# Kernel optimization log

Measured on AMD Instinct MI355X. Metric: run time of the kernel, lower is better.

The kernel has to match this reference:

```python
import jax, jax.numpy as jnp
import numpy as np

D = 512      # d_model
H = 8        # n_head
L = 6        # n_layers
DFF = 2048   # d_inner
V = 10000    # vocab
NPOS = 2048
B, T = 8, 1023
S = 1024     # encoder length


def sinusoid_table(n_position, d_hid):
    pos = np.arange(n_position)[:, None].astype(np.float64)
    i = np.arange(d_hid)[None, :]
    angle = pos / np.power(10000.0, 2 * (i // 2) / d_hid)
    tab = np.zeros((n_position, d_hid))
    tab[:, 0::2] = np.sin(angle[:, 0::2])
    tab[:, 1::2] = np.cos(angle[:, 1::2])
    return jnp.asarray(tab, jnp.float32)


def layer_norm(x, g, b, eps=1e-6):
    m = x.mean(-1, keepdims=True)
    v = x.var(-1, keepdims=True)
    return (x - m) / jnp.sqrt(v + eps) * g + b


def mha(x, kv, wq, wk, wv, wo, g, b, mask):
    # x: [B,Lq,D], kv: [B,Lk,D], mask: [B,Lq|1,Lk] int or None
    Bq, Lq, _ = x.shape
    Lk = kv.shape[1]
    dk = D // H
    q = (x @ wq).reshape(Bq, Lq, H, dk).transpose(0, 2, 1, 3)   # bhqd
    k = (kv @ wk).reshape(Bq, Lk, H, dk).transpose(0, 2, 1, 3)  # bhkd
    v = (kv @ wv).reshape(Bq, Lk, H, dk).transpose(0, 2, 1, 3)
    scores = jnp.einsum('bhqd,bhkd->bhqk', q, k) / jnp.sqrt(jnp.asarray(dk, x.dtype))
    if mask is not None:
        scores = jnp.where(mask[:, None, :, :] == 0, jnp.asarray(-1e9, x.dtype), scores)
    a = jax.nn.softmax(scores, axis=-1)
    o = jnp.einsum('bhqk,bhkd->bhqd', a, v).transpose(0, 2, 1, 3).reshape(Bq, Lq, D)
    o = o @ wo + x  # residual
    return layer_norm(o, g, b)


def ffn(x, w1, b1, w2, b2, g, b):
    h = jax.nn.relu(x @ w1 + b1)
    return layer_norm(h @ w2 + b2 + x, g, b)


def setup_inputs() -> dict:
    key = jax.random.key(0)
    ks = iter(jax.random.split(key, 64))
    sc = 0.02
    inp = {}
    inp['trg_seq'] = jax.random.randint(next(ks), (B, T), 0, V, dtype=jnp.int32)
    # causal mask over decoder length T+1 (1 = attend)
    T1 = T + 1
    inp['trg_mask'] = jnp.tril(jnp.ones((T1, T1), jnp.int32))[None].repeat(B, axis=0)
    inp['enc_output'] = jax.random.normal(next(ks), (B, S, D), jnp.float32)
    inp['src_mask'] = jnp.ones((B, 1, S), jnp.int32)
    inp['emb'] = jax.random.normal(next(ks), (V, D), jnp.float32) * sc
    inp['ln0_g'] = jnp.ones((D,), jnp.float32)
    inp['ln0_b'] = jnp.zeros((D,), jnp.float32)
    for nm in ['wq_s', 'wk_s', 'wv_s', 'wo_s', 'wq_c', 'wk_c', 'wv_c', 'wo_c']:
        inp[nm] = jax.random.normal(next(ks), (L, D, D), jnp.float32) * sc
    for nm in ['ln1_g', 'ln2_g', 'ln3_g']:
        inp[nm] = jnp.ones((L, D), jnp.float32)
    for nm in ['ln1_b', 'ln2_b', 'ln3_b']:
        inp[nm] = jnp.zeros((L, D), jnp.float32)
    inp['w1'] = jax.random.normal(next(ks), (L, D, DFF), jnp.float32) * sc
    inp['b1'] = jnp.zeros((L, DFF), jnp.float32)
    inp['w2'] = jax.random.normal(next(ks), (L, DFF, D), jnp.float32) * sc
    inp['b2'] = jnp.zeros((L, D), jnp.float32)
    return inp


def reference(trg_seq, trg_mask, enc_output, src_mask, emb, ln0_g, ln0_b,
              wq_s, wk_s, wv_s, wo_s, ln1_g, ln1_b,
              wq_c, wk_c, wv_c, wo_c, ln2_g, ln2_b,
              w1, b1, w2, b2, ln3_g, ln3_b):
    Bq, Tq = trg_seq.shape
    tok = emb[trg_seq]                                         # [B,T,D]
    x = jnp.concatenate([jnp.zeros((Bq, 1, D), tok.dtype), tok], axis=1)  # [B,T+1,D]
    x = x + sinusoid_table(NPOS, D)[None, :Tq + 1]
    x = layer_norm(x, ln0_g, ln0_b)
    for l in range(L):
        x = mha(x, x, wq_s[l], wk_s[l], wv_s[l], wo_s[l], ln1_g[l], ln1_b[l], trg_mask)
        x = mha(x, enc_output, wq_c[l], wk_c[l], wv_c[l], wo_c[l], ln2_g[l], ln2_b[l], src_mask)
        x = ffn(x, w1[l], b1[l], w2[l], b2[l], ln3_g[l], ln3_b[l])
    return x
```

## Files before the change

### kernel.cpp

```cpp
#include <hip/hip_runtime.h>
#include <stdint.h>


typedef unsigned short u16;
typedef float floatx4 __attribute__((ext_vector_type(4)));
typedef short short8 __attribute__((ext_vector_type(8)));

__device__ __forceinline__ float b2f(u16 u) {
    union { unsigned int i; float f; } c; c.i = ((unsigned int)u) << 16; return c.f;
}
__device__ __forceinline__ u16 f2b(float f) {
    union { float f; unsigned int i; } c; c.f = f;
    return (u16)((c.i + 0x7FFFu + ((c.i >> 16) & 1u)) >> 16);
}
__device__ __forceinline__ float ldf(const void* p, size_t i, bool is32) {
    return is32 ? ((const float*)p)[i] : b2f(((const u16*)p)[i]);
}
__device__ __forceinline__ void async16(u16* lds, const u16* g) {
    __builtin_amdgcn_global_load_lds(
        (const __attribute__((address_space(1))) unsigned int*)g,
        (__attribute__((address_space(3))) unsigned int*)lds, 16, 0, 0);
}
__device__ __forceinline__ void xcd_remap(int gx, int gy, int& bx, int& by) {
    const int fid = bx + gx * by;
    const int xcd = fid & 7;
    const int i = fid >> 3;
    bx = i % gx;
    by = xcd * (gy >> 3) + i / gx;
}

__global__ __launch_bounds__(256)
void conv_bf16_kernel(const void* __restrict__ src, u16* __restrict__ dst,
                      const u16* __restrict__ probe)
{
    const bool is32 = (probe[0] == 0);
    const size_t off = ((size_t)blockIdx.x * 256 + threadIdx.x) * 4;
    u16 o[4];
    if (is32) {
        float4 f = *(const float4*)((const float*)src + off);
        o[0] = f2b(f.x); o[1] = f2b(f.y); o[2] = f2b(f.z); o[3] = f2b(f.w);
    } else {
        uint2 vv = *(const uint2*)((const u16*)src + off);
        const u16* pv = (const u16*)&vv;
        o[0] = pv[0]; o[1] = pv[1]; o[2] = pv[2]; o[3] = pv[3];
    }
    *(uint2*)&dst[off] = *(uint2*)o;
}

__global__ __launch_bounds__(256)
void transpose_layer_kernel(const void* __restrict__ wq_s, const void* __restrict__ wk_s,
                            const void* __restrict__ wv_s, const void* __restrict__ wo_s,
                            const void* __restrict__ wq_c, const void* __restrict__ wk_c,
                            const void* __restrict__ wv_c, const void* __restrict__ wo_c,
                            const void* __restrict__ w1,   const void* __restrict__ w2,
                            u16* __restrict__ wT, const u16* __restrict__ probe,
                            size_t loff2, size_t loff1)
{
    __shared__ u16 tile[32][33];
    const bool is32 = (probe[0] == 0);
    const int bid = blockIdx.x;
    const int tid = threadIdx.x;
    const void* src; u16* dst; int C, R, tr, tc; size_t loff;
    if (bid < 2048) {
        const int mat = bid >> 8, t = bid & 255;
        R = 512; C = 512; tr = t >> 4; tc = t & 15; loff = loff2;
        const void* tbl[8] = {wq_s, wk_s, wv_s, wo_s, wq_c, wk_c, wv_c, wo_c};
        src = tbl[mat]; dst = wT + (size_t)mat * 262144;
    } else if (bid < 3072) {
        const int t = bid - 2048;
        R = 512; C = 2048; tr = t >> 6; tc = t & 63; loff = loff1;
        src = w1; dst = wT + 2097152;
    } else {
        const int t = bid - 3072;
        R = 2048; C = 512; tr = t >> 4; tc = t & 15; loff = loff1;
        src = w2; dst = wT + 3145728;
    }
    const int r = tid >> 3, c0 = (tid & 7) * 4;
    const size_t off = loff + (size_t)(tr * 32 + r) * C + tc * 32 + c0;
    u16 vals[4];
    if (is32) {
        float4 f = *(const float4*)((const float*)src + off);
        vals[0] = f2b(f.x); vals[1] = f2b(f.y); vals[2] = f2b(f.z); vals[3] = f2b(f.w);
    } else {
        uint2 vv = *(const uint2*)((const u16*)src + off);
        const u16* pv = (const u16*)&vv;
        vals[0] = pv[0]; vals[1] = pv[1]; vals[2] = pv[2]; vals[3] = pv[3];
    }
#pragma unroll
    for (int j = 0; j < 4; j++) tile[r][c0 + j] = vals[j];
    __syncthreads();
    uint2 ov; u16* po = (u16*)&ov;
#pragma unroll
    for (int j = 0; j < 4; j++) po[j] = tile[c0 + j][r];
    *(uint2*)&dst[(size_t)(tc * 32 + r) * R + tr * 32 + c0] = ov;
}

template<int EPI>
__global__ __launch_bounds__(512)
void gemm256(const u16* __restrict__ A, const u16* __restrict__ Bt,
             const void* __restrict__ bias, size_t boff,
             u16* __restrict__ outb, u16* __restrict__ out1, u16* __restrict__ out2,
             const u16* __restrict__ probe, int M, int N, int K)
{
    __shared__ u16 As[2][256 * 64];
    __shared__ u16 Bs[2][256 * 64];
    const int tid = threadIdx.x;
    const int lane = tid & 63;
    const int quad = lane >> 4, cl = lane & 15;
    const int wave = tid >> 6;
    const int wm2 = (wave >> 2) * 128;
    const int wn2 = (wave & 3) * 64;
    int bx = blockIdx.x, by = blockIdx.y;
    xcd_remap(gridDim.x, gridDim.y, bx, by);
    const int m0 = by * 256, n0 = bx * 256;

    floatx4 acc[8][4];
#pragma unroll
    for (int i = 0; i < 8; i++)
#pragma unroll
        for (int j = 0; j < 4; j++)
#pragma unroll
            for (int r = 0; r < 4; r++) acc[i][j][r] = 0.0f;

    const int lrow = lane >> 3;
    const int lcol = ((lane & 7) ^ lrow) * 8;
    const u16* gA = &A [(size_t)(m0 + wave * 8 + lrow) * K + lcol];
    const u16* gB = &Bt[(size_t)(n0 + wave * 8 + lrow) * K + lcol];

    auto stage = [&](int bsel, int k0) {
#pragma unroll
        for (int s = 0; s < 4; s++)
            async16(&As[bsel][(s * 64 + wave * 8) * 64], gA + (size_t)s * 64 * K + k0);
#pragma unroll
        for (int s = 0; s < 4; s++)
            async16(&Bs[bsel][(s * 64 + wave * 8) * 64], gB + (size_t)s * 64 * K + k0);
    };

    const int nkt = K >> 6;
    stage(0, 0);
    stage(1, 64);

    const int c7 = cl & 7;
    for (int t = 0; t < nkt; ++t) {
        const int cur = t & 1;
        if (t == nkt - 1) asm volatile("s_waitcnt vmcnt(0)" ::: "memory");
        else              asm volatile("s_waitcnt vmcnt(8)" ::: "memory");
        __builtin_amdgcn_sched_barrier(0);
        __builtin_amdgcn_s_barrier();

        const u16* Ac = As[cur];
        const u16* Bc = Bs[cur];
#pragma unroll
        for (int kk = 0; kk < 2; kk++) {
            const int gsw = ((kk * 4 + quad) ^ c7) * 8;
            short8 af[8], bf[4];
#pragma unroll
            for (int mi = 0; mi < 8; mi++)
                af[mi] = *(const short8*)&Ac[(wm2 + mi * 16 + cl) * 64 + gsw];
#pragma unroll
            for (int ni = 0; ni < 4; ni++)
                bf[ni] = *(const short8*)&Bc[(wn2 + ni * 16 + cl) * 64 + gsw];
#pragma unroll
            for (int mi = 0; mi < 8; mi++)
#pragma unroll
                for (int ni = 0; ni < 4; ni++)
                    acc[mi][ni] = __builtin_amdgcn_mfma_f32_16x16x32_bf16(af[mi], bf[ni], acc[mi][ni], 0, 0, 0);
        }
        __builtin_amdgcn_s_barrier();
        __builtin_amdgcn_sched_barrier(0);
        if (t + 2 < nkt) stage(cur, (t + 2) * 64);
    }

    if (EPI == 4 || EPI == 5) {
        const int sub = n0 >> 9;
        const int cbase = (n0 & 511) + wn2;
        const bool isV = (EPI == 4) ? (sub == 2) : (sub == 1);
        if (!isV) {
            u16* dst = (sub == 0) ? outb : out1;
#pragma unroll
            for (int mi = 0; mi < 8; mi++)
#pragma unroll
                for (int ni = 0; ni < 4; ni++) {
                    const int c = cbase + ni * 16 + cl;
#pragma unroll
                    for (int r = 0; r < 4; r++)
                        dst[(size_t)(m0 + wm2 + mi * 16 + quad * 4 + r) * 512 + c] = f2b(acc[mi][ni][r]);
                }
        } else {
            u16* dst = (EPI == 4) ? out2 : out1;
#pragma unroll
            for (int mi = 0; mi < 8; mi++) {
                const int row0 = m0 + wm2 + mi * 16 + quad * 4;
                const int b8 = (row0 >> 10) * 8;
                const int key0 = row0 & 1023;
#pragma unroll
                for (int ni = 0; ni < 4; ni++) {
                    const int c = cbase + ni * 16 + cl;
                    u16 pk[4];
#pragma unroll
                    for (int r = 0; r < 4; r++) pk[r] = f2b(acc[mi][ni][r]);
                    const size_t vrow = (size_t)(b8 + (c >> 6)) * 64 + (c & 63);
                    *(uint2*)&dst[vrow * 1024 + key0] = *(uint2*)pk;
                }
            }
        }
        return;
    }

    const bool is32 = (probe[0] == 0);
#pragma unroll
    for (int mi = 0; mi < 8; mi++) {
#pragma unroll
        for (int ni = 0; ni < 4; ni++) {
            const int col = n0 + wn2 + ni * 16 + cl;
            const float bv = ldf(bias, boff + col, is32);
#pragma unroll
            for (int r = 0; r < 4; r++) {
                const int row = m0 + wm2 + mi * 16 + quad * 4 + r;
                float v = acc[mi][ni][r] + bv;
                v = fmaxf(v, 0.0f);
                outb[(size_t)row * N + col] = f2b(v);
            }
        }
    }
}

template<int EPI>
__global__ __launch_bounds__(256)
void gemm_bf16(const u16* __restrict__ A, const u16* __restrict__ Bt,
               const void* __restrict__ bias, size_t boff, float* __restrict__ resid,
               u16* __restrict__ outb, u16* __restrict__ out1, u16* __restrict__ out2,
               const u16* __restrict__ probe, int M, int N, int K)
{
    __shared__ u16 As[3][128 * 32];
    __shared__ u16 Bs[3][128 * 32];
    const int tid = threadIdx.x;
    const int lane = tid & 63;
    const int quad = lane >> 4, cl = lane & 15;
    const int wave = tid >> 6;
    const int wm = (wave >> 1) * 64, wn = (wave & 1) * 64;
    int bx = blockIdx.x, by = blockIdx.y;
    xcd_remap(gridDim.x, gridDim.y, bx, by);
    const int m0 = by * 128, n0 = bx * 128;

    floatx4 acc[4][4];
#pragma unroll
    for (int i = 0; i < 4; i++)
#pragma unroll
        for (int j = 0; j < 4; j++)
#pragma unroll
            for (int r = 0; r < 4; r++) acc[i][j][r] = 0.0f;

    const int srow = tid >> 2;
    const int scol = (((tid & 3) ^ ((srow >> 1) & 3))) * 8;
    const int rslot = (quad ^ ((cl >> 1) & 3)) * 8;
    const int Ksub = K / gridDim.z;
    const int kbeg = blockIdx.z * Ksub, kend = kbeg + Ksub;
    const int nsteps = (kend - kbeg) >> 5;

    const u16* ga0 = &A [(size_t)(m0 + srow) * K + scol];
    const u16* ga1 = &A [(size_t)(m0 + 64 + srow) * K + scol];
    const u16* gb0 = &Bt[(size_t)(n0 + srow) * K + scol];
    const u16* gb1 = &Bt[(size_t)(n0 + 64 + srow) * K + scol];

    auto stage = [&](int bsel, int kk) {
        async16(&As[bsel][wave * 512],        ga0 + kk);
        async16(&As[bsel][2048 + wave * 512], ga1 + kk);
        async16(&Bs[bsel][wave * 512],        gb0 + kk);
        async16(&Bs[bsel][2048 + wave * 512], gb1 + kk);
    };

    stage(0, kbeg);
    if (nsteps > 1) stage(1, kbeg + 32);

    for (int t = 0; t < nsteps; ++t) {
        const int cur = t % 3;
        if (t + 2 < nsteps) stage((t + 2) % 3, kbeg + (t + 2) * 32);
        const int rem = nsteps - 1 - t;
        if (rem >= 2)      asm volatile("s_waitcnt vmcnt(8)" ::: "memory");
        else if (rem == 1) asm volatile("s_waitcnt vmcnt(4)" ::: "memory");
        else               asm volatile("s_waitcnt vmcnt(0)" ::: "memory");
        __builtin_amdgcn_sched_barrier(0);
        __builtin_amdgcn_s_barrier();

        const u16* Ac = As[cur];
        const u16* Bc = Bs[cur];
        short8 af[4], bfr[4];
#pragma unroll
        for (int mi = 0; mi < 4; mi++) af[mi]  = *(const short8*)&Ac[(wm + mi * 16 + cl) * 32 + rslot];
#pragma unroll
        for (int ni = 0; ni < 4; ni++) bfr[ni] = *(const short8*)&Bc[(wn + ni * 16 + cl) * 32 + rslot];
#pragma unroll
        for (int mi = 0; mi < 4; mi++)
#pragma unroll
            for (int ni = 0; ni < 4; ni++)
                acc[mi][ni] = __builtin_amdgcn_mfma_f32_16x16x32_bf16(af[mi], bfr[ni], acc[mi][ni], 0, 0, 0);
        __builtin_amdgcn_s_barrier();
    }

    bool is32 = false;
    if (EPI == 1 || EPI == 2 || EPI == 3) is32 = (probe[0] == 0);
    const bool addbias = (bias != nullptr) && (blockIdx.z == 0);
    float* pslice = (EPI == 3) ? resid + (size_t)blockIdx.z * M * N : resid;
#pragma unroll
    for (int mi = 0; mi < 4; mi++) {
#pragma unroll
        for (int ni = 0; ni < 4; ni++) {
            const int col = n0 + wn + ni * 16 + cl;
#pragma unroll
            for (int r = 0; r < 4; r++) {
                const int row = m0 + wm + mi * 16 + quad * 4 + r;
                float v = acc[mi][ni][r];
                if (EPI == 1) { v += ldf(bias, boff + col, is32); v = fmaxf(v, 0.0f); }
                if (EPI == 2) {
                    if (addbias) v += ldf(bias, boff + col, is32);
                    atomicAdd(&resid[(size_t)row * N + col], v);
                } else if (EPI == 3) {
                    if (addbias) v += ldf(bias, boff + col, is32);
                    pslice[(size_t)row * N + col] = v;
                } else {
                    outb[(size_t)row * N + col] = f2b(v);
                }
            }
        }
    }
}

template<int CAUSAL>
__global__ __launch_bounds__(256)
void attn_kernel(const u16* __restrict__ Q, const u16* __restrict__ Kb,
                 const u16* __restrict__ VT, u16* __restrict__ O)
{
    __shared__ u16 Kt[64][72];
    __shared__ u16 Vt[64][72];
    int qt = blockIdx.x, bh = blockIdx.y;
    xcd_remap(gridDim.x, gridDim.y, qt, bh);
    const int b = bh >> 3, h = bh & 7;
    const int tid = threadIdx.x;
    const int w = tid >> 6;
    const int lane = tid & 63;
    const int quad = lane >> 4, cl = lane & 15;

    const size_t qrow = (size_t)(b * 1024 + qt * 64 + w * 16 + cl) * 512 + h * 64;
    const short8 qf0 = *(const short8*)&Q[qrow + quad * 8];
    const short8 qf1 = *(const short8*)&Q[qrow + 32 + quad * 8];
    const int qg = qt * 64 + w * 16 + cl;

    float lsum = 0.0f;
    floatx4 oacc[4];
#pragma unroll
    for (int nb = 0; nb < 4; nb++)
#pragma unroll
        for (int r = 0; r < 4; r++) oacc[nb][r] = 0.0f;

    const int trow = tid >> 3, tcol = (tid & 7) * 8;
    const int tv = tid & 7;
    const int vm = (tv >> 2) * 32 + (tv & 1) * 16 + ((tv >> 1) & 1) * 4;
    const size_t kbase = (size_t)(b * 1024) * 512 + h * 64;
    const size_t vbase = (size_t)(bh * 64) * 1024;

    const int nkt = CAUSAL ? (qt + 1) : 16;
    uint4 ka0 = *(const uint4*)&Kb[kbase + (size_t)trow * 512 + tcol];
    uint4 ka1 = *(const uint4*)&Kb[kbase + (size_t)(trow + 32) * 512 + tcol];
    uint4 va0 = *(const uint4*)&VT[vbase + (size_t)trow * 1024 + tcol];
    uint4 va1 = *(const uint4*)&VT[vbase + (size_t)(trow + 32) * 1024 + tcol];

    for (int kt = 0; kt < nkt; kt++) {
        *(uint4*)&Kt[trow][tcol]      = ka0;
        *(uint4*)&Kt[trow + 32][tcol] = ka1;
        *(uint2*)&Vt[trow][vm]          = make_uint2(va0.x, va0.y);
        *(uint2*)&Vt[trow][vm + 8]      = make_uint2(va0.z, va0.w);
        *(uint2*)&Vt[trow + 32][vm]     = make_uint2(va1.x, va1.y);
        *(uint2*)&Vt[trow + 32][vm + 8] = make_uint2(va1.z, va1.w);
        if (kt + 1 < nkt) {
            const int k1 = (kt + 1) * 64;
            ka0 = *(const uint4*)&Kb[kbase + (size_t)(k1 + trow) * 512 + tcol];
            ka1 = *(const uint4*)&Kb[kbase + (size_t)(k1 + trow + 32) * 512 + tcol];
            va0 = *(const uint4*)&VT[vbase + (size_t)trow * 1024 + k1 + tcol];
            va1 = *(const uint4*)&VT[vbase + (size_t)(trow + 32) * 1024 + k1 + tcol];
        }
        asm volatile("s_waitcnt lgkmcnt(0)" ::: "memory");
        __builtin_amdgcn_sched_barrier(0);
        __builtin_amdgcn_s_barrier();
        __builtin_amdgcn_sched_barrier(0);

        const int k0 = kt * 64;
        floatx4 sacc[4];
#pragma unroll
        for (int kb2 = 0; kb2 < 4; kb2++)
#pragma unroll
            for (int r = 0; r < 4; r++) sacc[kb2][r] = 0.0f;
#pragma unroll
        for (int kb2 = 0; kb2 < 4; kb2++) {
            const short8 kf0 = *(const short8*)&Kt[kb2 * 16 + cl][quad * 8];
            const short8 kf1 = *(const short8*)&Kt[kb2 * 16 + cl][32 + quad * 8];
            sacc[kb2] = __builtin_amdgcn_mfma_f32_16x16x32_bf16(kf0, qf0, sacc[kb2], 0, 0, 0);
            sacc[kb2] = __builtin_amdgcn_mfma_f32_16x16x32_bf16(kf1, qf1, sacc[kb2], 0, 0, 0);
        }
        const bool need_mask = CAUSAL && (kt == nkt - 1);
        float p[4][4];
#pragma unroll
        for (int kb2 = 0; kb2 < 4; kb2++) {
#pragma unroll
            for (int r = 0; r < 4; r++) {
                float e = __expf(sacc[kb2][r] * 0.125f);
                if (need_mask) {
                    const int key = k0 + kb2 * 16 + quad * 4 + r;
                    e = (key > qg) ? 0.0f : e;
                }
                p[kb2][r] = e;
                lsum += e;
            }
        }
        unsigned int pk[4][2];
#pragma unroll
        for (int kb2 = 0; kb2 < 4; kb2++) {
            asm("v_cvt_pk_bf16_f32 %0, %1, %2" : "=v"(pk[kb2][0]) : "v"(p[kb2][0]), "v"(p[kb2][1]));
            asm("v_cvt_pk_bf16_f32 %0, %1, %2" : "=v"(pk[kb2][1]) : "v"(p[kb2][2]), "v"(p[kb2][3]));
        }
#pragma unroll
        for (int c = 0; c < 2; c++) {
            union { short8 s8; unsigned int u[4]; } pa;
            pa.u[0] = pk[2 * c][0];     pa.u[1] = pk[2 * c][1];
            pa.u[2] = pk[2 * c + 1][0]; pa.u[3] = pk[2 * c + 1][1];
#pragma unroll
            for (int nb = 0; nb < 4; nb++) {
                const short8 vf = *(const short8*)&Vt[nb * 16 + cl][c * 32 + quad * 8];
                oacc[nb] = __builtin_amdgcn_mfma_f32_16x16x32_bf16(pa.s8, vf, oacc[nb], 0, 0, 0);
            }
        }
        __builtin_amdgcn_sched_barrier(0);
        __builtin_amdgcn_s_barrier();
        __builtin_amdgcn_sched_barrier(0);
    }
    lsum += __shfl_xor(lsum, 16, 64);
    lsum += __shfl_xor(lsum, 32, 64);
    float inv[4];
#pragma unroll
    for (int r = 0; r < 4; r++) inv[r] = 1.0f / __shfl(lsum, quad * 4 + r, 64);
#pragma unroll
    for (int nb = 0; nb < 4; nb++) {
#pragma unroll
        for (int r = 0; r < 4; r++) {
            const float v = oacc[nb][r] * inv[r];
            O[(size_t)(b * 1024 + qt * 64 + w * 16 + quad * 4 + r) * 512 + h * 64 + nb * 16 + cl] = f2b(v);
        }
    }
}

__device__ __forceinline__ float2 block_ln_512(float v0, float v1,
                                               float g0, float g1, float b0, float b1,
                                               int tid)
{
    __shared__ float red[8];
    float s = v0 + v1, sq = v0 * v0 + v1 * v1;
#pragma unroll
    for (int m = 1; m < 64; m <<= 1) { s += __shfl_xor(s, m, 64); sq += __shfl_xor(sq, m, 64); }
    const int wv = tid >> 6;
    if ((tid & 63) == 0) { red[wv * 2] = s; red[wv * 2 + 1] = sq; }
    __syncthreads();
    s  = red[0] + red[2] + red[4] + red[6];
    sq = red[1] + red[3] + red[5] + red[7];
    const float mean = s * (1.0f / 512.0f);
    const float var = sq * (1.0f / 512.0f) - mean * mean;
    const float rstd = rsqrtf(var + 1e-6f);
    return make_float2((v0 - mean) * rstd * g0 + b0, (v1 - mean) * rstd * g1 + b1);
}

__global__ __launch_bounds__(256)
void ln_kernel(float* __restrict__ xf, const void* __restrict__ g, const void* __restrict__ bb,
               size_t goff, const u16* __restrict__ probe,
               u16* __restrict__ xb, void* __restrict__ finalout,
               const float* __restrict__ p0, const float* __restrict__ p1)
{
    const bool is32 = (probe[0] == 0);
    const int row = blockIdx.x, tid = threadIdx.x;
    const int i = tid * 2;
    const size_t base = (size_t)row * 512;
    float2 v = *(const float2*)&xf[base + i];
    if (p0) {
        const float2 a = *(const float2*)&p0[base + i];
        const float2 b = *(const float2*)&p1[base + i];
        v.x += a.x + b.x;
        v.y += a.y + b.y;
    }
    const float2 y = block_ln_512(v.x, v.y, ldf(g, goff + i, is32), ldf(g, goff + i + 1, is32),
                                  ldf(bb, goff + i, is32), ldf(bb, goff + i + 1, is32), tid);
    if (finalout) {
        if (is32) {
            *(float2*)&((float*)finalout)[base + i] = y;
        } else {
            u16* ob = (u16*)finalout;
            ob[base + i] = f2b(y.x); ob[base + i + 1] = f2b(y.y);
        }
    } else {
        *(float2*)&xf[base + i] = y;
        xb[base + i] = f2b(y.x); xb[base + i + 1] = f2b(y.y);
    }
}

__global__ __launch_bounds__(256)
void embed_ln_kernel(const int* __restrict__ trg_seq, const void* __restrict__ emb,
                     const void* __restrict__ g, const void* __restrict__ bb,
                     const u16* __restrict__ probe,
                     float* __restrict__ xf, u16* __restrict__ xb)
{
    const bool is32 = (probe[0] == 0);
    const int row = blockIdx.x;
    const int b = row >> 10, t = row & 1023;
    const int tid = threadIdx.x;
    const int tok = (t == 0) ? -1 : trg_seq[b * 1023 + t - 1];
    const int i = tid * 2;
    const float freq = __expf((float)i * (-9.210340371976184f / 512.0f));
    const float angle = (float)t * freq;
    float v0 = sinf(angle), v1 = cosf(angle);
    if (tok >= 0) {
        v0 += ldf(emb, (size_t)tok * 512 + i, is32);
        v1 += ldf(emb, (size_t)tok * 512 + i + 1, is32);
    }
    const float2 y = block_ln_512(v0, v1, ldf(g, i, is32), ldf(g, i + 1, is32),
                                  ldf(bb, i, is32), ldf(bb, i + 1, is32), tid);
    const size_t base = (size_t)row * 512;
    *(float2*)&xf[base + i] = y;
    xb[base + i] = f2b(y.x); xb[base + i + 1] = f2b(y.y);
}

extern "C" void kernel_launch(void* const* d_in, const int* in_sizes, int n_in,
                              void* d_out, int out_size, void* d_ws, size_t ws_size,
                              hipStream_t stream)
{
    const int* trg_seq = (const int*)d_in[0];
    const void* enc   = d_in[2];
    const void* emb   = d_in[4];
    const void* ln0_g = d_in[5];
    const void* ln0_b = d_in[6];
    const u16* probe  = (const u16*)d_in[5];

    char* ws = (char*)d_ws;
    float* xf   = (float*)(ws);
    u16*   xb   = (u16*)  (ws + (16u << 20));
    u16*   qb   = (u16*)  (ws + (24u << 20));
    u16*   kb   = (u16*)  (ws + (32u << 20));
    u16*   vt   = (u16*)  (ws + (40u << 20));
    u16*   ao   = (u16*)  (ws + (48u << 20));
    u16*   hb   = (u16*)  (ws + (24u << 20));
    u16*   wT   = (u16*)  (ws + (56u << 20));
    u16*   encb = (u16*)  (ws + (64u << 20));
    const bool bigws = ws_size >= (108ull << 20);
    float* p0 = (float*)(ws + (72u << 20));
    float* p1 = (float*)(ws + (88u << 20));
    const float* lp0 = bigws ? p0 : nullptr;
    const float* lp1 = bigws ? p1 : nullptr;

    const size_t E2 = 262144, E1 = 1048576;
    const dim3 gqkv(6, 32), gkv(4, 32), gffn1(8, 32);
    const dim3 g512(4, 64);
    const dim3 g512s(4, 64, 2), gffn2(4, 64, 2), gattn(16, 64);

    conv_bf16_kernel<<<4096, 256, 0, stream>>>(enc, encb, probe);
    embed_ln_kernel<<<8192, 256, 0, stream>>>(trg_seq, emb, ln0_g, ln0_b, probe, xf, xb);

    for (int l = 0; l < 6; l++) {
        transpose_layer_kernel<<<4096, 256, 0, stream>>>(
            d_in[7], d_in[8], d_in[9], d_in[10], d_in[11], d_in[12], d_in[13], d_in[14],
            d_in[21], d_in[23], wT, probe, (size_t)l * E2, (size_t)l * E1);

        gemm256<4><<<gqkv, 512, 0, stream>>>(xb, wT, nullptr, 0,
                                             qb, kb, vt, probe, 8192, 1536, 512);
        attn_kernel<1><<<gattn, 256, 0, stream>>>(qb, kb, vt, ao);
        if (bigws)
            gemm_bf16<3><<<g512s, 256, 0, stream>>>(ao, wT + 3 * E2, nullptr, 0, p0,
                                                    nullptr, nullptr, nullptr, probe, 8192, 512, 512);
        else
            gemm_bf16<2><<<g512s, 256, 0, stream>>>(ao, wT + 3 * E2, nullptr, 0, xf,
                                                    nullptr, nullptr, nullptr, probe, 8192, 512, 512);
        ln_kernel<<<8192, 256, 0, stream>>>(xf, d_in[15], d_in[18], (size_t)l * 512, probe, xb,
                                            nullptr, lp0, lp1);

        gemm_bf16<0><<<g512, 256, 0, stream>>>(xb, wT + 4 * E2, nullptr, 0, nullptr,
                                               qb, nullptr, nullptr, probe, 8192, 512, 512);
        gemm256<5><<<gkv, 512, 0, stream>>>(encb, wT + 5 * E2, nullptr, 0,
                                            kb, vt, nullptr, probe, 8192, 1024, 512);
        attn_kernel<0><<<gattn, 256, 0, stream>>>(qb, kb, vt, ao);
        if (bigws)
            gemm_bf16<3><<<g512s, 256, 0, stream>>>(ao, wT + 7 * E2, nullptr, 0, p0,
                                                    nullptr, nullptr, nullptr, probe, 8192, 512, 512);
        else
            gemm_bf16<2><<<g512s, 256, 0, stream>>>(ao, wT + 7 * E2, nullptr, 0, xf,
                                                    nullptr, nullptr, nullptr, probe, 8192, 512, 512);
        ln_kernel<<<8192, 256, 0, stream>>>(xf, d_in[16], d_in[19], (size_t)l * 512, probe, xb,
                                            nullptr, lp0, lp1);

        gemm256<1><<<gffn1, 512, 0, stream>>>(xb, wT + 2097152, d_in[22], (size_t)l * 2048,
                                              hb, nullptr, nullptr, probe, 8192, 2048, 512);
        if (bigws)
            gemm_bf16<3><<<gffn2, 256, 0, stream>>>(hb, wT + 3145728, d_in[24], (size_t)l * 512, p0,
                                                    nullptr, nullptr, nullptr, probe, 8192, 512, 2048);
        else
            gemm_bf16<2><<<gffn2, 256, 0, stream>>>(hb, wT + 3145728, d_in[24], (size_t)l * 512, xf,
                                                    nullptr, nullptr, nullptr, probe, 8192, 512, 2048);
        ln_kernel<<<8192, 256, 0, stream>>>(xf, d_in[17], d_in[20], (size_t)l * 512, probe, xb,
                                            (l == 5) ? d_out : nullptr, lp0, lp1);
    }
}
```

Baseline: 1.797 ms.

## Fuse cross-attn Q and KV projections into one 128-tile GEMM launch

```diff
diff --git a/kernel.cpp b/kernel.cpp
--- a/kernel.cpp
+++ b/kernel.cpp
@@ -171,42 +171,6 @@
         if (t + 2 < nkt) stage(cur, (t + 2) * 64);
     }
 
-    if (EPI == 4 || EPI == 5) {
-        const int sub = n0 >> 9;
-        const int cbase = (n0 & 511) + wn2;
-        const bool isV = (EPI == 4) ? (sub == 2) : (sub == 1);
-        if (!isV) {
-            u16* dst = (sub == 0) ? outb : out1;
-#pragma unroll
-            for (int mi = 0; mi < 8; mi++)
-#pragma unroll
-                for (int ni = 0; ni < 4; ni++) {
-                    const int c = cbase + ni * 16 + cl;
-#pragma unroll
-                    for (int r = 0; r < 4; r++)
-                        dst[(size_t)(m0 + wm2 + mi * 16 + quad * 4 + r) * 512 + c] = f2b(acc[mi][ni][r]);
-                }
-        } else {
-            u16* dst = (EPI == 4) ? out2 : out1;
-#pragma unroll
-            for (int mi = 0; mi < 8; mi++) {
-                const int row0 = m0 + wm2 + mi * 16 + quad * 4;
-                const int b8 = (row0 >> 10) * 8;
-                const int key0 = row0 & 1023;
-#pragma unroll
-                for (int ni = 0; ni < 4; ni++) {
-                    const int c = cbase + ni * 16 + cl;
-                    u16 pk[4];
-#pragma unroll
-                    for (int r = 0; r < 4; r++) pk[r] = f2b(acc[mi][ni][r]);
-                    const size_t vrow = (size_t)(b8 + (c >> 6)) * 64 + (c & 63);
-                    *(uint2*)&dst[vrow * 1024 + key0] = *(uint2*)pk;
-                }
-            }
-        }
-        return;
-    }
-
     const bool is32 = (probe[0] == 0);
 #pragma unroll
     for (int mi = 0; mi < 8; mi++) {
@@ -243,6 +207,12 @@
     xcd_remap(gridDim.x, gridDim.y, bx, by);
     const int m0 = by * 128, n0 = bx * 128;
 
+    const u16* Ause = A;
+    if (EPI == 4) {
+        const u16* A2 = (const u16*)bias;
+        if (A2 != nullptr && n0 >= 512) Ause = A2;
+    }
+
     floatx4 acc[4][4];
 #pragma unroll
     for (int i = 0; i < 4; i++)
@@ -258,8 +228,8 @@
     const int kbeg = blockIdx.z * Ksub, kend = kbeg + Ksub;
     const int nsteps = (kend - kbeg) >> 5;
 
-    const u16* ga0 = &A [(size_t)(m0 + srow) * K + scol];
-    const u16* ga1 = &A [(size_t)(m0 + 64 + srow) * K + scol];
+    const u16* ga0 = &Ause[(size_t)(m0 + srow) * K + scol];
+    const u16* ga1 = &Ause[(size_t)(m0 + 64 + srow) * K + scol];
     const u16* gb0 = &Bt[(size_t)(n0 + srow) * K + scol];
     const u16* gb1 = &Bt[(size_t)(n0 + 64 + srow) * K + scol];
 
@@ -296,6 +266,41 @@
             for (int ni = 0; ni < 4; ni++)
                 acc[mi][ni] = __builtin_amdgcn_mfma_f32_16x16x32_bf16(af[mi], bfr[ni], acc[mi][ni], 0, 0, 0);
         __builtin_amdgcn_s_barrier();
+    }
+
+    if (EPI == 4) {
+        const int seg = n0 >> 9;
+        const int cbase = (n0 & 511) + wn;
+        if (seg < 2) {
+            u16* dst = (seg == 0) ? outb : out1;
+#pragma unroll
+            for (int mi = 0; mi < 4; mi++)
+#pragma unroll
+                for (int ni = 0; ni < 4; ni++) {
+                    const int c = cbase + ni * 16 + cl;
+#pragma unroll
+                    for (int r = 0; r < 4; r++)
+                        dst[(size_t)(m0 + wm + mi * 16 + quad * 4 + r) * 512 + c] = f2b(acc[mi][ni][r]);
+                }
+        } else {
+            u16* dst = out2;
+#pragma unroll
+            for (int mi = 0; mi < 4; mi++) {
+                const int row0 = m0 + wm + mi * 16 + quad * 4;
+                const int b8 = (row0 >> 10) * 8;
+                const int key0 = row0 & 1023;
+#pragma unroll
+                for (int ni = 0; ni < 4; ni++) {
+                    const int c = cbase + ni * 16 + cl;
+                    u16 pk[4];
+#pragma unroll
+                    for (int r = 0; r < 4; r++) pk[r] = f2b(acc[mi][ni][r]);
+                    const size_t vrow = (size_t)(b8 + (c >> 6)) * 64 + (c & 63);
+                    *(uint2*)&dst[vrow * 1024 + key0] = *(uint2*)pk;
+                }
+            }
+        }
+        return;
     }
 
     bool is32 = false;
@@ -480,9 +485,11 @@
     float2 v = *(const float2*)&xf[base + i];
     if (p0) {
         const float2 a = *(const float2*)&p0[base + i];
+        v.x += a.x; v.y += a.y;
+    }
+    if (p1) {
         const float2 b = *(const float2*)&p1[base + i];
-        v.x += a.x + b.x;
-        v.y += a.y + b.y;
+        v.x += b.x; v.y += b.y;
     }
     const float2 y = block_ln_512(v.x, v.y, ldf(g, goff + i, is32), ldf(g, goff + i + 1, is32),
                                   ldf(bb, goff + i, is32), ldf(bb, goff + i + 1, is32), tid);
@@ -553,9 +560,10 @@
     const float* lp1 = bigws ? p1 : nullptr;
 
     const size_t E2 = 262144, E1 = 1048576;
-    const dim3 gqkv(6, 32), gkv(4, 32), gffn1(8, 32);
-    const dim3 g512(4, 64);
-    const dim3 g512s(4, 64, 2), gffn2(4, 64, 2), gattn(16, 64);
+    const dim3 gqkv(12, 64);
+    const dim3 gffn1(8, 32);
+    const dim3 gproj(4, 64);
+    const dim3 gffn2(4, 64, 2), gattn(16, 64);
 
     conv_bf16_kernel<<<4096, 256, 0, stream>>>(enc, encb, probe);
     embed_ln_kernel<<<8192, 256, 0, stream>>>(trg_seq, emb, ln0_g, ln0_b, probe, xf, xb);
@@ -565,31 +573,29 @@
             d_in[7], d_in[8], d_in[9], d_in[10], d_in[11], d_in[12], d_in[13], d_in[14],
             d_in[21], d_in[23], wT, probe, (size_t)l * E2, (size_t)l * E1);
 
-        gemm256<4><<<gqkv, 512, 0, stream>>>(xb, wT, nullptr, 0,
-                                             qb, kb, vt, probe, 8192, 1536, 512);
+        gemm_bf16<4><<<gqkv, 256, 0, stream>>>(xb, wT, xb, 0, nullptr,
+                                               qb, kb, vt, probe, 8192, 1536, 512);
         attn_kernel<1><<<gattn, 256, 0, stream>>>(qb, kb, vt, ao);
         if (bigws)
-            gemm_bf16<3><<<g512s, 256, 0, stream>>>(ao, wT + 3 * E2, nullptr, 0, p0,
+            gemm_bf16<3><<<gproj, 256, 0, stream>>>(ao, wT + 3 * E2, nullptr, 0, p0,
                                                     nullptr, nullptr, nullptr, probe, 8192, 512, 512);
         else
-            gemm_bf16<2><<<g512s, 256, 0, stream>>>(ao, wT + 3 * E2, nullptr, 0, xf,
+            gemm_bf16<2><<<gproj, 256, 0, stream>>>(ao, wT + 3 * E2, nullptr, 0, xf,
                                                     nullptr, nullptr, nullptr, probe, 8192, 512, 512);
         ln_kernel<<<8192, 256, 0, stream>>>(xf, d_in[15], d_in[18], (size_t)l * 512, probe, xb,
-                                            nullptr, lp0, lp1);
-
-        gemm_bf16<0><<<g512, 256, 0, stream>>>(xb, wT + 4 * E2, nullptr, 0, nullptr,
-                                               qb, nullptr, nullptr, probe, 8192, 512, 512);
-        gemm256<5><<<gkv, 512, 0, stream>>>(encb, wT + 5 * E2, nullptr, 0,
-                                            kb, vt, nullptr, probe, 8192, 1024, 512);
+                                            nullptr, lp0, nullptr);
+
+        gemm_bf16<4><<<gqkv, 256, 0, stream>>>(xb, wT + 4 * E2, encb, 0, nullptr,
+                                               qb, kb, vt, probe, 8192, 1536, 512);
         attn_kernel<0><<<gattn, 256, 0, stream>>>(qb, kb, vt, ao);
         if (bigws)
-            gemm_bf16<3><<<g512s, 256, 0, stream>>>(ao, wT + 7 * E2, nullptr, 0, p0,
+            gemm_bf16<3><<<gproj, 256, 0, stream>>>(ao, wT + 7 * E2, nullptr, 0, p0,
                                                     nullptr, nullptr, nullptr, probe, 8192, 512, 512);
         else
-            gemm_bf16<2><<<g512s, 256, 0, stream>>>(ao, wT + 7 * E2, nullptr, 0, xf,
+            gemm_bf16<2><<<gproj, 256, 0, stream>>>(ao, wT + 7 * E2, nullptr, 0, xf,
                                                     nullptr, nullptr, nullptr, probe, 8192, 512, 512);
         ln_kernel<<<8192, 256, 0, stream>>>(xf, d_in[16], d_in[19], (size_t)l * 512, probe, xb,
-                                            nullptr, lp0, lp1);
+                                            nullptr, lp0, nullptr);
 
         gemm256<1><<<gffn1, 512, 0, stream>>>(xb, wT + 2097152, d_in[22], (size_t)l * 2048,
                                               hb, nullptr, nullptr, probe, 8192, 2048, 512);
```

After: 1.637 ms. 1.1x faster.
